# Kernel optimization log

Measured on AMD Instinct MI355X. Metric: run time of the kernel, lower is better.

The kernel has to match this reference:

```python
import jax, jax.numpy as jnp
import numpy as np
from jax import lax

# data_spacing = (dx, dy, dz) matched to spatial axes (1, 2, 3) of (B, S, R, C)
SPACING = (2.0, 1.5, 1.5)


def _pad_edge(X, axis):
    pad = [(0, 0)] * X.ndim
    pad[axis] = (1, 1)
    return jnp.pad(X, pad, mode='edge')  # torch ReplicationPad equivalent


def _dc(X, axis, d):
    # central difference with replication padding: (X[i+1]-X[i-1])/(2d)
    Xp = _pad_edge(X, axis)
    n = X.shape[axis]
    return (lax.slice_in_dim(Xp, 2, n + 2, axis=axis)
            - lax.slice_in_dim(Xp, 0, n, axis=axis)) / (2.0 * d)


def _df(X, axis, d):
    # forward difference: (X[i+1]-X[i])/d
    Xp = _pad_edge(X, axis)
    n = X.shape[axis]
    return (lax.slice_in_dim(Xp, 2, n + 2, axis=axis)
            - lax.slice_in_dim(Xp, 1, n + 1, axis=axis)) / d


def _db(X, axis, d):
    # backward difference: (X[i]-X[i-1])/d
    Xp = _pad_edge(X, axis)
    n = X.shape[axis]
    return (lax.slice_in_dim(Xp, 1, n + 1, axis=axis)
            - lax.slice_in_dim(Xp, 0, n, axis=axis)) / d


def _set_bc_neumann(X):
    # crop 1-voxel boundary, then replicate-pad it back (Neumann / zero-flux BC)
    inner = X[:, 1:-1, 1:-1, 1:-1]
    return jnp.pad(inner, ((0, 0), (1, 1), (1, 1), (1, 1)), mode='edge')


def setup_inputs() -> dict:
    key = jax.random.key(0)
    k1, k2, k3 = jax.random.split(key, 3)
    B, S, R, C = 8, 128, 192, 192
    t = jax.random.normal(k1, (B,), dtype=jnp.float32)
    batch_P = jax.random.normal(k2, (B, S, R, C), dtype=jnp.float32)
    D = jax.random.uniform(k3, (B, S, R, C), dtype=jnp.float32)  # scalar diffusivity field
    return {"t": t, "batch_P": batch_P, "D": D}


def reference(t, batch_P, D):
    P = _set_bc_neumann(batch_P)
    dx, dy, dz = SPACING
    # F = |grad P|^2 via central differences
    F = (_dc(P, 1, dx) ** 2 + _dc(P, 2, dy) ** 2 + _dc(P, 3, dz) ** 2)
    # G = laplacian P via backward(forward) differences per axis
    G = (_db(_df(P, 1, dx), 1, dx)
         + _db(_df(P, 2, dy), 2, dy)
         + _db(_df(P, 3, dz), 3, dz))
    # dP/dt = -1/2 |grad P|^2 - D * laplacian P
    return -0.5 * F - D * G
```

## Files before the change

kernel.cpp:

```cpp
#include <hip/hip_runtime.h>


#define BB 8
#define SS 128
#define RR 192
#define CC 192

__device__ __forceinline__ int clamp1(int x, int hi) {
    return min(max(x, 1), hi);
}

__global__ __launch_bounds__(256) void flowp_kernel(
    const float* __restrict__ P,
    const float* __restrict__ D,
    float* __restrict__ out)
{
    const float inv2dx = 0.25f;
    const float inv2dy = 1.0f / 3.0f;
    const float inv2dz = 1.0f / 3.0f;
    const float invdx2 = 0.25f;
    const float invdy2 = 1.0f / 2.25f;
    const float invdz2 = 1.0f / 2.25f;

    const int total = BB * SS * RR * CC;
    int idx = blockIdx.x * blockDim.x + threadIdx.x;
    if (idx >= total) return;

    int k  = idx % CC;
    int t1 = idx / CC;
    int j  = t1 % RR;
    int t2 = t1 / RR;
    int i  = t2 % SS;
    int b  = t2 / SS;

    const int ci  = clamp1(i,     SS - 2);
    const int cim = clamp1(i - 1, SS - 2);
    const int cip = clamp1(i + 1, SS - 2);
    const int cj  = clamp1(j,     RR - 2);
    const int cjm = clamp1(j - 1, RR - 2);
    const int cjp = clamp1(j + 1, RR - 2);
    const int ck  = clamp1(k,     CC - 2);
    const int ckm = clamp1(k - 1, CC - 2);
    const int ckp = clamp1(k + 1, CC - 2);

    const int bo = b * SS;
    const int rowc = ((bo + ci) * RR + cj) * CC;

    const float pc  = P[rowc + ck];
    const float pCm = P[rowc + ckm];
    const float pCp = P[rowc + ckp];
    const float pSm = P[((bo + cim) * RR + cj) * CC + ck];
    const float pSp = P[((bo + cip) * RR + cj) * CC + ck];
    const float pRm = P[((bo + ci) * RR + cjm) * CC + ck];
    const float pRp = P[((bo + ci) * RR + cjp) * CC + ck];

    const float dcx = (pSp - pSm) * inv2dx;
    const float dcy = (pRp - pRm) * inv2dy;
    const float dcz = (pCp - pCm) * inv2dz;
    const float F = dcx * dcx + dcy * dcy + dcz * dcz;

    const float G = (pSp - 2.0f * pc + pSm) * invdx2
                  + (pRp - 2.0f * pc + pRm) * invdy2
                  + (pCp - 2.0f * pc + pCm) * invdz2;

    const float d = D[idx];
    out[idx] = -0.5f * F - d * G;
}

extern "C" void kernel_launch(void* const* d_in, const int* in_sizes, int n_in,
                              void* d_out, int out_size, void* d_ws, size_t ws_size,
                              hipStream_t stream) {
    const float* P = (const float*)d_in[1];
    const float* D = (const float*)d_in[2];
    float* out = (float*)d_out;

    const int total = BB * SS * RR * CC;
    const int threads = 256;
    const int blocks = (total + threads - 1) / threads;
    flowp_kernel<<<blocks, threads, 0, stream>>>(P, D, out);
}
```

Baseline: 370.2 us.

## Vectorize stencil to float4 per thread with 3D grid and nontemporal I/O

Each thread now computes four consecutive points along the contiguous axis using 128-bit vector loads for the center and neighbour rows, handling edge clamping with lane selects. A 3D grid removes the per-thread integer division and modulo index decode. D is read and the output written with nontemporal hints to avoid polluting cache. This cuts load instruction count and address arithmetic, but adds edge-case select logic and a fixed block shape tied to the problem dimensions.

```diff
diff --git a/kernel.cpp b/kernel.cpp
--- a/kernel.cpp
+++ b/kernel.cpp
@@ -6,14 +6,11 @@
 #define RR 192
 #define CC 192
 
-__device__ __forceinline__ int clamp1(int x, int hi) {
-    return min(max(x, 1), hi);
-}
+typedef float v4f __attribute__((ext_vector_type(4)));
 
-__global__ __launch_bounds__(256) void flowp_kernel(
-    const float* __restrict__ P,
-    const float* __restrict__ D,
-    float* __restrict__ out)
+__device__ __forceinline__ float stencil_pt(float pc, float pSm, float pSp,
+                                            float pRm, float pRp,
+                                            float pCm, float pCp, float d)
 {
     const float inv2dx = 0.25f;
     const float inv2dy = 1.0f / 3.0f;
@@ -22,49 +19,74 @@
     const float invdy2 = 1.0f / 2.25f;
     const float invdz2 = 1.0f / 2.25f;
 
-    const int total = BB * SS * RR * CC;
-    int idx = blockIdx.x * blockDim.x + threadIdx.x;
-    if (idx >= total) return;
+    float dcx = (pSp - pSm) * inv2dx;
+    float dcy = (pRp - pRm) * inv2dy;
+    float dcz = (pCp - pCm) * inv2dz;
+    float F = dcx * dcx + dcy * dcy + dcz * dcz;
+    float G = (pSp - 2.0f * pc + pSm) * invdx2
+            + (pRp - 2.0f * pc + pRm) * invdy2
+            + (pCp - 2.0f * pc + pCm) * invdz2;
+    return -0.5f * F - d * G;
+}
 
-    int k  = idx % CC;
-    int t1 = idx / CC;
-    int j  = t1 % RR;
-    int t2 = t1 / RR;
-    int i  = t2 % SS;
-    int b  = t2 / SS;
+__global__ __launch_bounds__(192) void flowp_kernel(
+    const float* __restrict__ P,
+    const float* __restrict__ D,
+    float* __restrict__ out)
+{
+    const int tx = threadIdx.x;
+    const int k0 = tx << 2;
+    const int j  = blockIdx.y * 4 + threadIdx.y;
+    const int bz = blockIdx.z;
+    const int i  = bz & (SS - 1);
+    const int b  = bz >> 7;
 
-    const int ci  = clamp1(i,     SS - 2);
-    const int cim = clamp1(i - 1, SS - 2);
-    const int cip = clamp1(i + 1, SS - 2);
-    const int cj  = clamp1(j,     RR - 2);
-    const int cjm = clamp1(j - 1, RR - 2);
-    const int cjp = clamp1(j + 1, RR - 2);
-    const int ck  = clamp1(k,     CC - 2);
-    const int ckm = clamp1(k - 1, CC - 2);
-    const int ckp = clamp1(k + 1, CC - 2);
+    const int ci  = min(max(i,     1), SS - 2);
+    const int cim = min(max(i - 1, 1), SS - 2);
+    const int cip = min(max(i + 1, 1), SS - 2);
+    const int cj  = min(max(j,     1), RR - 2);
+    const int cjm = min(max(j - 1, 1), RR - 2);
+    const int cjp = min(max(j + 1, 1), RR - 2);
 
-    const int bo = b * SS;
-    const int rowc = ((bo + ci) * RR + cj) * CC;
+    const int bS = b * SS;
+    const int rowC  = ((bS + ci ) * RR + cj ) * CC;
+    const int rowSm = ((bS + cim) * RR + cj ) * CC;
+    const int rowSp = ((bS + cip) * RR + cj ) * CC;
+    const int rowRm = ((bS + ci ) * RR + cjm) * CC;
+    const int rowRp = ((bS + ci ) * RR + cjp) * CC;
 
-    const float pc  = P[rowc + ck];
-    const float pCm = P[rowc + ckm];
-    const float pCp = P[rowc + ckp];
-    const float pSm = P[((bo + cim) * RR + cj) * CC + ck];
-    const float pSp = P[((bo + cip) * RR + cj) * CC + ck];
-    const float pRm = P[((bo + ci) * RR + cjm) * CC + ck];
-    const float pRp = P[((bo + ci) * RR + cjp) * CC + ck];
+    const bool e0 = (tx == 0);
+    const bool e1 = (tx == 47);
 
-    const float dcx = (pSp - pSm) * inv2dx;
-    const float dcy = (pRp - pRm) * inv2dy;
-    const float dcz = (pCp - pCm) * inv2dz;
-    const float F = dcx * dcx + dcy * dcy + dcz * dcz;
+    const v4f c4 = *(const v4f*)(P + rowC + k0);
+    const int cmI = e0 ? 1      : k0 - 1;
+    const int cpI = e1 ? CC - 2 : k0 + 4;
+    const float cm = P[rowC + cmI];
+    const float cp = P[rowC + cpI];
+    const float w1 = e0 ? c4.y : c4.x;
+    const float w2 = c4.y;
+    const float w3 = c4.z;
+    const float w4 = e1 ? c4.z : c4.w;
 
-    const float G = (pSp - 2.0f * pc + pSm) * invdx2
-                  + (pRp - 2.0f * pc + pRm) * invdy2
-                  + (pCp - 2.0f * pc + pCm) * invdz2;
+    v4f nSm = *(const v4f*)(P + rowSm + k0);
+    v4f nSp = *(const v4f*)(P + rowSp + k0);
+    v4f nRm = *(const v4f*)(P + rowRm + k0);
+    v4f nRp = *(const v4f*)(P + rowRp + k0);
+    nSm.x = e0 ? nSm.y : nSm.x;  nSm.w = e1 ? nSm.z : nSm.w;
+    nSp.x = e0 ? nSp.y : nSp.x;  nSp.w = e1 ? nSp.z : nSp.w;
+    nRm.x = e0 ? nRm.y : nRm.x;  nRm.w = e1 ? nRm.z : nRm.w;
+    nRp.x = e0 ? nRp.y : nRp.x;  nRp.w = e1 ? nRp.z : nRp.w;
 
-    const float d = D[idx];
-    out[idx] = -0.5f * F - d * G;
+    const int idxO = ((bS + i) * RR + j) * CC + k0;
+    const v4f d4 = __builtin_nontemporal_load((const v4f*)(D + idxO));
+
+    v4f o;
+    o.x = stencil_pt(w1, nSm.x, nSp.x, nRm.x, nRp.x, cm, w2, d4.x);
+    o.y = stencil_pt(w2, nSm.y, nSp.y, nRm.y, nRp.y, w1, w3, d4.y);
+    o.z = stencil_pt(w3, nSm.z, nSp.z, nRm.z, nRp.z, w2, w4, d4.z);
+    o.w = stencil_pt(w4, nSm.w, nSp.w, nRm.w, nRp.w, w3, cp, d4.w);
+
+    __builtin_nontemporal_store(o, (v4f*)(out + idxO));
 }
 
 extern "C" void kernel_launch(void* const* d_in, const int* in_sizes, int n_in,
@@ -74,8 +96,7 @@
     const float* D = (const float*)d_in[2];
     float* out = (float*)d_out;
 
-    const int total = BB * SS * RR * CC;
-    const int threads = 256;
-    const int blocks = (total + threads - 1) / threads;
-    flowp_kernel<<<blocks, threads, 0, stream>>>(P, D, out);
+    dim3 block(48, 4, 1);
+    dim3 grid(1, RR / 4, BB * SS);
+    flowp_kernel<<<grid, block, 0, stream>>>(P, D, out);
 }
```

Measured after the change: 341.4 us. 7.8% less time.
